# Kernel tuning notes

Hardware: AMD Instinct MI355X
Metric: run time of the kernel (lower is better)

Reference implementation:

```python
import jax, jax.numpy as jnp
import numpy as np

C = 256
CQ = C // 4


def setup_inputs() -> dict:
    key = jax.random.key(0)
    ks = jax.random.split(key, 7)
    B, H, W = 4, 64, 64
    x = jax.random.normal(ks[0], (B, C, H, W), dtype=jnp.float32)
    s = 1.0 / np.sqrt(C)
    Wq = jax.random.normal(ks[1], (CQ, C), dtype=jnp.float32) * s
    bq = jnp.zeros((CQ,), dtype=jnp.float32)
    Wk = jax.random.normal(ks[2], (CQ, C), dtype=jnp.float32) * s
    bk = jnp.zeros((CQ,), dtype=jnp.float32)
    Wv = jax.random.normal(ks[3], (C, C), dtype=jnp.float32) * s
    bv = jnp.zeros((C,), dtype=jnp.float32)
    gamma = jnp.zeros((1,), dtype=jnp.float32)
    return {"x": x, "Wq": Wq, "bq": bq, "Wk": Wk, "bk": bk,
            "Wv": Wv, "bv": bv, "gamma": gamma}


def reference(x, Wq, bq, Wk, bk, Wv, bv, gamma):
    B, Cc, Hh, Ww = x.shape
    N = Hh * Ww
    xf = x.reshape(B, Cc, N)                      # [B, C, N]
    # 1x1 convs are channel-mixing matmuls
    q = jnp.einsum('oc,bcn->bon', Wq, xf) + bq[None, :, None]   # [B, C/4, N]
    k = jnp.einsum('oc,bcn->bon', Wk, xf) + bk[None, :, None]   # [B, C/4, N]
    v = jnp.einsum('oc,bcn->bon', Wv, xf) + bv[None, :, None]   # [B, C, N]
    energy = jnp.einsum('bci,bcj->bij', q, k)     # [B, N, N] (unscaled)
    attn = jax.nn.softmax(energy, axis=-1)
    out = jnp.einsum('bcj,bij->bci', v, attn)     # [B, C, N]
    out = out.reshape(B, Cc, Hh, Ww)
    return gamma[0] * out + x
```

## Files before the change

kernel.cpp:

```cpp
#include <hip/hip_runtime.h>
#include <hip/hip_bf16.h>

typedef unsigned short u16;
typedef unsigned int u32;
typedef float f32x4 __attribute__((ext_vector_type(4)));
typedef short s16x8 __attribute__((ext_vector_type(8)));
typedef short s16x4 __attribute__((ext_vector_type(4)));

#define MFMA16(a, b, c) __builtin_amdgcn_mfma_f32_16x16x32_bf16(a, b, c, 0, 0, 0)

#define NN 4096
#define CC 256
#define CQ 64

__device__ __forceinline__ u16 f2bf(float x) {
    union { float f; u32 u; } v; v.f = x;
    return (u16)((v.u + 0x7FFFu + ((v.u >> 16) & 1u)) >> 16);
}
__device__ __forceinline__ float bf2f(u16 u) {
    union { u32 u; float f; } v; v.u = ((u32)u) << 16;
    return v.f;
}
__device__ __forceinline__ void gll16(const void* g, void* l) {
    __builtin_amdgcn_global_load_lds(
        (const __attribute__((address_space(1))) void*)g,
        (__attribute__((address_space(3))) void*)l, 16, 0, 0);
}

__global__ __launch_bounds__(256) void prep(
    const float* __restrict__ x, const float* __restrict__ Wq,
    const float* __restrict__ Wk, const float* __restrict__ Wv,
    u16* __restrict__ xT, u16* __restrict__ wbf)
{
    const int bid = blockIdx.x, t = threadIdx.x;
    if (bid < 1024) {
        __shared__ float tile[64 * 65];
        const int b = bid >> 8, ctile = (bid >> 6) & 3, ntile = bid & 63;
        const int c0 = ctile * 64, n0 = ntile * 64;
        const int cw = t >> 4, nj = (t & 15) * 4;
        for (int it = 0; it < 4; it++) {
            const int ci = it * 16 + cw;
            const float4 v4 = *(const float4*)(x + ((size_t)(b * CC + c0 + ci)) * NN + n0 + nj);
            tile[(nj + 0) * 65 + ci] = v4.x;
            tile[(nj + 1) * 65 + ci] = v4.y;
            tile[(nj + 2) * 65 + ci] = v4.z;
            tile[(nj + 3) * 65 + ci] = v4.w;
        }
        __syncthreads();
        const int r = t >> 2, c16 = (t & 3) * 16;
        union { u16 h[16]; uint4 q[2]; } pk;
        for (int j = 0; j < 16; j++) pk.h[j] = f2bf(tile[r * 65 + c16 + j]);
        u16* dst = xT + ((size_t)(b * NN + n0 + r)) * CC + c0 + c16;
        *(uint4*)dst = pk.q[0];
        *(uint4*)(dst + 8) = pk.q[1];
    } else {
        const int flat = (bid - 1024) * 1024 + t * 4;
        const int o = flat >> 8, c = flat & 255;
        const float* src = (o < 64)  ? (Wq + (size_t)o * CC + c)
                         : (o < 128) ? (Wk + (size_t)(o - 64) * CC + c)
                                     : (Wv + (size_t)(o - 128) * CC + c);
        const float4 v4 = *(const float4*)src;
        union { u16 h[4]; uint2 d; } pk;
        pk.h[0] = f2bf(v4.x); pk.h[1] = f2bf(v4.y);
        pk.h[2] = f2bf(v4.z); pk.h[3] = f2bf(v4.w);
        *(uint2*)(wbf + (size_t)o * CC + c) = pk.d;
    }
}

__global__ __launch_bounds__(256, 2) void qkv(
    const u16* __restrict__ xT, const u16* __restrict__ wbf,
    const float* __restrict__ bq, const float* __restrict__ bk,
    const float* __restrict__ bv,
    u16* __restrict__ qT, u16* __restrict__ kT, u16* __restrict__ v)
{
    __shared__ __align__(16) u16 sm[384 * 64 + 32 * 64];
    u16* Ws = sm;
    u16* Xs = sm + 384 * 64;

    const int bid = blockIdx.x;
    const int b = bid >> 7, n0 = (bid & 127) * 32;
    const int t = threadIdx.x, lane = t & 63, w = t >> 6;
    const int col = lane & 15, quad = lane >> 4;

    f32x4 acc[6][2];
    for (int i = 0; i < 6; i++) { acc[i][0] = f32x4{0,0,0,0}; acc[i][1] = f32x4{0,0,0,0}; }

    for (int cc = 0; cc < 4; cc++) {
        const int c0 = cc * 64;
        for (int m = 0; m < 12; m++) {
            const int g = w * 768 + m * 64 + lane;
            const int row = g >> 3, ch = g & 7;
            gll16(wbf + (size_t)row * CC + c0 + ((ch ^ (row & 7)) * 8),
                  Ws + (size_t)(w * 768 + m * 64) * 8 + lane * 8);
        }
        {
            const int g = w * 64 + lane;
            const int n = g >> 3, ch = g & 7;
            gll16(xT + ((size_t)(b * NN + n0 + n)) * CC + c0 + ((ch ^ (n & 7)) * 8),
                  Xs + (size_t)(w * 64) * 8 + lane * 8);
        }
        __syncthreads();
        for (int kk = 0; kk < 2; kk++) {
            s16x8 bx[2];
            for (int nt2 = 0; nt2 < 2; nt2++) {
                const int n = nt2 * 16 + col;
                bx[nt2] = *(const s16x8*)&Xs[n * 64 + (((kk * 4 + quad) ^ (n & 7)) * 8)];
            }
            for (int ot = 0; ot < 6; ot++) {
                const int row = w * 96 + ot * 16 + col;
                const s16x8 a = *(const s16x8*)&Ws[row * 64 + (((kk * 4 + quad) ^ (row & 7)) * 8)];
                acc[ot][0] = MFMA16(a, bx[0], acc[ot][0]);
                acc[ot][1] = MFMA16(a, bx[1], acc[ot][1]);
            }
        }
        __syncthreads();
    }
    for (int ot = 0; ot < 6; ot++) {
        const int og = w * 96 + ot * 16 + quad * 4;
        for (int nt2 = 0; nt2 < 2; nt2++) {
            const int n = n0 + nt2 * 16 + col;
            if (og < 64) {
                union { u16 h[4]; uint2 d; } pk;
                for (int r = 0; r < 4; r++) pk.h[r] = f2bf(acc[ot][nt2][r] + bq[og + r]);
                *(uint2*)(qT + ((size_t)(b * NN + n)) * CQ + og) = pk.d;
            } else if (og < 128) {
                union { u16 h[4]; uint2 d; } pk;
                for (int r = 0; r < 4; r++) pk.h[r] = f2bf(acc[ot][nt2][r] + bk[og - 64 + r]);
                *(uint2*)(kT + ((size_t)(b * NN + n)) * CQ + (og - 64)) = pk.d;
            } else {
                for (int r = 0; r < 4; r++)
                    v[((size_t)(b * CC + og - 128 + r)) * NN + n] =
                        f2bf(acc[ot][nt2][r] + bv[og - 128 + r]);
            }
        }
    }
}

__global__ __launch_bounds__(512, 2) void flash_attn(
    const u16* __restrict__ qT, const u16* __restrict__ kT,
    const u16* __restrict__ v, const float* __restrict__ x,
    const float* __restrict__ gamma, float* __restrict__ out)
{
    __shared__ __align__(16) u16 sm[49664];
    __shared__ float ls[2][64];

    const int bid = blockIdx.x;
    const int p = bid & 7;
    const int b = p >> 1;
    const int n0 = ((bid >> 3) + (p & 1) * 32) * 64;
    const int t = threadIdx.x;
    const int lane = t & 63, wv = t >> 6;
    const int col = lane & 15, quad = lane >> 4;
    const int strip = wv & 3, jhalf = wv >> 2;
    const int ih = wv >> 2, cq = wv & 3;

    s16x8 aq[2];
    {
        const u16* qp = qT + ((size_t)(b * NN + n0 + strip * 16 + col)) * CQ + quad * 8;
        aq[0] = *(const s16x8*)qp;
        aq[1] = *(const s16x8*)(qp + 32);
    }

    f32x4 o_[2][4];
    for (int i = 0; i < 2; i++) for (int j = 0; j < 4; j++) o_[i][j] = f32x4{0,0,0,0};
    float l[4] = {0.f, 0.f, 0.f, 0.f};

    const int kg = wv * 64 + lane;
    const int krow = kg >> 3;
    const u16* ksrc = kT + ((size_t)(b * NN + krow)) * CQ + (((kg & 7) ^ (krow & 7)) * 8);
    const int kdo = kg * 8;
    int vgi[4];
    const u16* vsrc[4];
    for (int m = 0; m < 4; m++) {
        const int g = wv * 256 + m * 64 + lane;
        const int row = g >> 3;
        vgi[m] = g * 8;
        vsrc[m] = v + ((size_t)(b * CC + row)) * NN + (((g & 7) ^ (row & 7)) * 8);
    }

    auto issueK = [&](int jt, int kb) {
        gll16(ksrc + (size_t)jt * 64 * CQ, sm + kb * 4096 + kdo);
    };
    auto issueV = [&](int jt, int vb) {
        u16* base = sm + 8192 + vb * 16384;
        for (int m = 0; m < 4; m++)
            gll16(vsrc[m] + jt * 64, base + vgi[m]);
    };
    auto S_phase = [&](int kb, int pb) {
        const u16* Kb = sm + kb * 4096;
        u16* Pb = sm + 40960 + pb * 4352;
        f32x4 s[2] = { f32x4{0,0,0,0}, f32x4{0,0,0,0} };
        for (int kk = 0; kk < 2; kk++)
            for (int jtt = 0; jtt < 2; jtt++) {
                const int jrow = jhalf * 32 + jtt * 16 + col;
                const s16x8 bk_ = *(const s16x8*)
                    &Kb[jrow * 64 + (((kk * 4 + quad) ^ (jrow & 7)) * 8)];
                s[jtt] = MFMA16(aq[kk], bk_, s[jtt]);
            }
        for (int jtt = 0; jtt < 2; jtt++)
            for (int r = 0; r < 4; r++) {
                const float pv = __expf(fminf(s[jtt][r], 60.f));
                l[r] += pv;
                Pb[(strip * 16 + quad * 4 + r) * 68 + jhalf * 32 + jtt * 16 + col] = f2bf(pv);
            }
    };
    auto PV_phase = [&](int pb, int vb) {
        const u16* Pb = sm + 40960 + pb * 4352;
        const u16* Vb = sm + 8192 + vb * 16384;
        for (int kk = 0; kk < 2; kk++) {
            s16x8 pa[2];
            for (int it2 = 0; it2 < 2; it2++) {
                const u16* pp = &Pb[((ih * 2 + it2) * 16 + col) * 68 + kk * 32 + quad * 8];
                const s16x4 lo = *(const s16x4*)pp;
                const s16x4 hi = *(const s16x4*)(pp + 4);
                pa[it2] = s16x8{lo[0], lo[1], lo[2], lo[3], hi[0], hi[1], hi[2], hi[3]};
            }
            for (int ct = 0; ct < 4; ct++) {
                const int c = cq * 64 + ct * 16 + col;
                const s16x8 bv_ = *(const s16x8*)
                    &Vb[c * 64 + (((kk * 4 + quad) ^ (c & 7)) * 8)];
                o_[0][ct] = MFMA16(pa[0], bv_, o_[0][ct]);
                o_[1][ct] = MFMA16(pa[1], bv_, o_[1][ct]);
            }
        }
    };

    issueK(0, 0);
    issueV(0, 0);
    issueK(1, 1);
    __syncthreads();
    S_phase(0, 0);

    int vcur = 0, pcur = 0;
    for (int m = 0; m < 64; m++) {
        __syncthreads();
        issueV((m + 1 < 64) ? m + 1 : 63, vcur ^ 1);
        issueK((m + 2 < 64) ? m + 2 : 63, m & 1);
        PV_phase(pcur, vcur);
        if (m < 63) S_phase((m + 1) & 1, pcur ^ 1);
        vcur ^= 1; pcur ^= 1;
    }

    for (int r = 0; r < 4; r++) {
        float lv = l[r];
        lv += __shfl_xor(lv, 1, 64);
        lv += __shfl_xor(lv, 2, 64);
        lv += __shfl_xor(lv, 4, 64);
        lv += __shfl_xor(lv, 8, 64);
        l[r] = lv;
    }
    if (col == 0)
        for (int r = 0; r < 4; r++)
            ls[jhalf][strip * 16 + quad * 4 + r] = l[r];
    __syncthreads();

    const float g = gamma[0];
    u16* Ts = sm;
    for (int it2 = 0; it2 < 2; it2++) {
        float sc[4];
        for (int r = 0; r < 4; r++) {
            const int irow = (ih * 2 + it2) * 16 + quad * 4 + r;
            sc[r] = g / (ls[0][irow] + ls[1][irow]);
        }
        for (int ct = 0; ct < 4; ct++) {
            const int c = cq * 64 + ct * 16 + col;
            union { u16 h[4]; uint2 d; } pk;
            for (int r = 0; r < 4; r++) pk.h[r] = f2bf(o_[it2][ct][r] * sc[r]);
            *(uint2*)&Ts[c * 72 + (ih * 2 + it2) * 16 + quad * 4] = pk.d;
        }
    }
    __syncthreads();
    for (int it = 0; it < 4; it++) {
        const int c = (t >> 3) + it * 64;
        const int n8 = (t & 7) * 8;
        const u16* os = &Ts[c * 72 + n8];
        const float* xp = x + ((size_t)(b * CC + c)) * NN + n0 + n8;
        float* op = out + ((size_t)(b * CC + c)) * NN + n0 + n8;
        const float4 x0 = *(const float4*)xp;
        const float4 x1 = *(const float4*)(xp + 4);
        float4 r0, r1;
        r0.x = x0.x + bf2f(os[0]); r0.y = x0.y + bf2f(os[1]);
        r0.z = x0.z + bf2f(os[2]); r0.w = x0.w + bf2f(os[3]);
        r1.x = x1.x + bf2f(os[4]); r1.y = x1.y + bf2f(os[5]);
        r1.z = x1.z + bf2f(os[6]); r1.w = x1.w + bf2f(os[7]);
        *(float4*)op = r0;
        *(float4*)(op + 4) = r1;
    }
}

extern "C" void kernel_launch(void* const* d_in, const int* in_sizes, int n_in,
                              void* d_out, int out_size, void* d_ws, size_t ws_size,
                              hipStream_t stream)
{
    const float* x     = (const float*)d_in[0];
    const float* Wq    = (const float*)d_in[1];
    const float* bq    = (const float*)d_in[2];
    const float* Wk    = (const float*)d_in[3];
    const float* bk    = (const float*)d_in[4];
    const float* Wv    = (const float*)d_in[5];
    const float* bv    = (const float*)d_in[6];
    const float* gamma = (const float*)d_in[7];
    float* out = (float*)d_out;

    u16* xT  = (u16*)d_ws;
    u16* wbf = xT  + (size_t)4 * NN * CC;
    u16* qTw = wbf + (size_t)384 * CC;
    u16* kTw = qTw + (size_t)4 * NN * CQ;
    u16* vw  = kTw + (size_t)4 * NN * CQ;

    prep<<<1120, 256, 0, stream>>>(x, Wq, Wk, Wv, xT, wbf);
    qkv<<<512, 256, 0, stream>>>(xT, wbf, bq, bk, bv, qTw, kTw, vw);
    flash_attn<<<256, 512, 0, stream>>>(qTw, kTw, vw, x, gamma, out);
}
```

Baseline: 185.7 us.

## Keep P in registers by transposing S and splitting keys across waves

Reorganizes the attention loop so each wave computes the transposed score tile (keys by queries). The exp'd probabilities then sit directly in the B-operand layout of a 16x16x16 MFMA, which removes the P round-trip through shared memory and one barrier per tile. Key columns are split across four waves, so partial outputs and row sums have to be reduced through shared memory in a serialized four-step epilogue. Other changes: simpler double buffering, a larger accumulator set (32 f32x4 per wave), an fp32 epilogue instead of bf16, and dropping the 2-blocks-per-CU launch bound, which risks lower occupancy.

```diff
diff --git a/kernel.cpp b/kernel.cpp
--- a/kernel.cpp
+++ b/kernel.cpp
@@ -9,6 +9,19 @@
 
 #define MFMA16(a, b, c) __builtin_amdgcn_mfma_f32_16x16x32_bf16(a, b, c, 0, 0, 0)
 
+__device__ __forceinline__ f32x4 mfma_k16(s16x4 a, s16x4 b, f32x4 c) {
+#if __has_builtin(__builtin_amdgcn_mfma_f32_16x16x16_bf16)
+    return __builtin_amdgcn_mfma_f32_16x16x16_bf16(a, b, c, 0, 0, 0);
+#elif __has_builtin(__builtin_amdgcn_mfma_f32_16x16x16bf16_1k)
+    return __builtin_amdgcn_mfma_f32_16x16x16bf16_1k(a, b, c, 0, 0, 0);
+#else
+    f32x4 d;
+    asm volatile("s_nop 1\n\tv_mfma_f32_16x16x16_bf16 %0, %1, %2, %3\n\ts_nop 1"
+                 : "=v"(d) : "v"(a), "v"(b), "v"(c));
+    return d;
+#endif
+}
+
 #define NN 4096
 #define CC 256
 #define CQ 64
@@ -16,10 +29,6 @@
 __device__ __forceinline__ u16 f2bf(float x) {
     union { float f; u32 u; } v; v.f = x;
     return (u16)((v.u + 0x7FFFu + ((v.u >> 16) & 1u)) >> 16);
-}
-__device__ __forceinline__ float bf2f(u16 u) {
-    union { u32 u; float f; } v; v.u = ((u32)u) << 16;
-    return v.f;
 }
 __device__ __forceinline__ void gll16(const void* g, void* l) {
     __builtin_amdgcn_global_load_lds(
@@ -136,13 +145,14 @@
     }
 }
 
-__global__ __launch_bounds__(512, 2) void flash_attn(
+__global__ __launch_bounds__(512) void flash_attn(
     const u16* __restrict__ qT, const u16* __restrict__ kT,
     const u16* __restrict__ v, const float* __restrict__ x,
     const float* __restrict__ gamma, float* __restrict__ out)
 {
-    __shared__ __align__(16) u16 sm[49664];
-    __shared__ float ls[2][64];
+    __shared__ __align__(16) u16 sm[40960];
+    __shared__ __align__(16) float ls[4][64];
+    __shared__ __align__(16) float linv[64];
 
     const int bid = blockIdx.x;
     const int p = bid & 7;
@@ -151,30 +161,28 @@
     const int t = threadIdx.x;
     const int lane = t & 63, wv = t >> 6;
     const int col = lane & 15, quad = lane >> 4;
-    const int strip = wv & 3, jhalf = wv >> 2;
-    const int ih = wv >> 2, cq = wv & 3;
-
-    s16x8 aq[2];
-    {
-        const u16* qp = qT + ((size_t)(b * NN + n0 + strip * 16 + col)) * CQ + quad * 8;
-        aq[0] = *(const s16x8*)qp;
-        aq[1] = *(const s16x8*)(qp + 32);
-    }
-
-    f32x4 o_[2][4];
-    for (int i = 0; i < 2; i++) for (int j = 0; j < 4; j++) o_[i][j] = f32x4{0,0,0,0};
-    float l[4] = {0.f, 0.f, 0.f, 0.f};
-
-    const int kg = wv * 64 + lane;
-    const int krow = kg >> 3;
-    const u16* ksrc = kT + ((size_t)(b * NN + krow)) * CQ + (((kg & 7) ^ (krow & 7)) * 8);
-    const int kdo = kg * 8;
-    int vgi[4];
+    const int jq = wv & 3, ch = wv >> 2;
+
+    s16x8 qfrag[4][2];
+    for (int it = 0; it < 4; it++) {
+        const u16* qp = qT + ((size_t)(b * NN + n0 + it * 16 + col)) * CQ + quad * 8;
+        qfrag[it][0] = *(const s16x8*)qp;
+        qfrag[it][1] = *(const s16x8*)(qp + 32);
+    }
+
+    f32x4 o_[8][4];
+    for (int i = 0; i < 8; i++) for (int j = 0; j < 4; j++) o_[i][j] = f32x4{0,0,0,0};
+    float lac[4] = {0.f, 0.f, 0.f, 0.f};
+
+    const int krow = t >> 3;
+    const u16* ksrc = kT + ((size_t)(b * NN + krow)) * CQ + (((t & 7) ^ (krow & 7)) * 8);
+    const int kdo = t * 8;
     const u16* vsrc[4];
+    int vdo[4];
     for (int m = 0; m < 4; m++) {
-        const int g = wv * 256 + m * 64 + lane;
+        const int g = m * 512 + t;
         const int row = g >> 3;
-        vgi[m] = g * 8;
+        vdo[m] = g * 8;
         vsrc[m] = v + ((size_t)(b * CC + row)) * NN + (((g & 7) ^ (row & 7)) * 8);
     }
 
@@ -184,105 +192,93 @@
     auto issueV = [&](int jt, int vb) {
         u16* base = sm + 8192 + vb * 16384;
         for (int m = 0; m < 4; m++)
-            gll16(vsrc[m] + jt * 64, base + vgi[m]);
-    };
-    auto S_phase = [&](int kb, int pb) {
-        const u16* Kb = sm + kb * 4096;
-        u16* Pb = sm + 40960 + pb * 4352;
-        f32x4 s[2] = { f32x4{0,0,0,0}, f32x4{0,0,0,0} };
-        for (int kk = 0; kk < 2; kk++)
-            for (int jtt = 0; jtt < 2; jtt++) {
-                const int jrow = jhalf * 32 + jtt * 16 + col;
-                const s16x8 bk_ = *(const s16x8*)
-                    &Kb[jrow * 64 + (((kk * 4 + quad) ^ (jrow & 7)) * 8)];
-                s[jtt] = MFMA16(aq[kk], bk_, s[jtt]);
-            }
-        for (int jtt = 0; jtt < 2; jtt++)
-            for (int r = 0; r < 4; r++) {
-                const float pv = __expf(fminf(s[jtt][r], 60.f));
-                l[r] += pv;
-                Pb[(strip * 16 + quad * 4 + r) * 68 + jhalf * 32 + jtt * 16 + col] = f2bf(pv);
-            }
-    };
-    auto PV_phase = [&](int pb, int vb) {
-        const u16* Pb = sm + 40960 + pb * 4352;
-        const u16* Vb = sm + 8192 + vb * 16384;
-        for (int kk = 0; kk < 2; kk++) {
-            s16x8 pa[2];
-            for (int it2 = 0; it2 < 2; it2++) {
-                const u16* pp = &Pb[((ih * 2 + it2) * 16 + col) * 68 + kk * 32 + quad * 8];
-                const s16x4 lo = *(const s16x4*)pp;
-                const s16x4 hi = *(const s16x4*)(pp + 4);
-                pa[it2] = s16x8{lo[0], lo[1], lo[2], lo[3], hi[0], hi[1], hi[2], hi[3]};
-            }
-            for (int ct = 0; ct < 4; ct++) {
-                const int c = cq * 64 + ct * 16 + col;
-                const s16x8 bv_ = *(const s16x8*)
-                    &Vb[c * 64 + (((kk * 4 + quad) ^ (c & 7)) * 8)];
-                o_[0][ct] = MFMA16(pa[0], bv_, o_[0][ct]);
-                o_[1][ct] = MFMA16(pa[1], bv_, o_[1][ct]);
-            }
-        }
+            gll16(vsrc[m] + jt * 64, base + vdo[m]);
     };
 
     issueK(0, 0);
     issueV(0, 0);
-    issueK(1, 1);
     __syncthreads();
-    S_phase(0, 0);
-
-    int vcur = 0, pcur = 0;
+
+    const int c8 = col & 7;
     for (int m = 0; m < 64; m++) {
-        __syncthreads();
-        issueV((m + 1 < 64) ? m + 1 : 63, vcur ^ 1);
-        issueK((m + 2 < 64) ? m + 2 : 63, m & 1);
-        PV_phase(pcur, vcur);
-        if (m < 63) S_phase((m + 1) & 1, pcur ^ 1);
-        vcur ^= 1; pcur ^= 1;
-    }
-
-    for (int r = 0; r < 4; r++) {
-        float lv = l[r];
-        lv += __shfl_xor(lv, 1, 64);
-        lv += __shfl_xor(lv, 2, 64);
-        lv += __shfl_xor(lv, 4, 64);
-        lv += __shfl_xor(lv, 8, 64);
-        l[r] = lv;
-    }
-    if (col == 0)
-        for (int r = 0; r < 4; r++)
-            ls[jhalf][strip * 16 + quad * 4 + r] = l[r];
+        const int cur = m & 1;
+        if (m < 63) { issueK(m + 1, cur ^ 1); issueV(m + 1, cur ^ 1); }
+
+        const u16* Kb = sm + cur * 4096;
+        f32x4 s[4];
+        for (int it = 0; it < 4; it++) s[it] = f32x4{0,0,0,0};
+        for (int kk = 0; kk < 2; kk++) {
+            const s16x8 a = *(const s16x8*)
+                &Kb[(jq * 16 + col) * 64 + (((kk * 4 + quad) ^ c8) * 8)];
+            for (int it = 0; it < 4; it++)
+                s[it] = MFMA16(a, qfrag[it][kk], s[it]);
+        }
+        s16x4 pfrag[4];
+        for (int it = 0; it < 4; it++) {
+            union { u16 h[4]; s16x4 v4; } pk;
+            for (int r = 0; r < 4; r++) {
+                const float pv = __expf(fminf(s[it][r], 60.f));
+                lac[it] += pv;
+                pk.h[r] = f2bf(pv);
+            }
+            pfrag[it] = pk.v4;
+        }
+        const u16* Vb = sm + 8192 + cur * 16384;
+        const int lch = jq * 2 + (quad >> 1), sub = (quad & 1) * 4;
+        for (int ct = 0; ct < 8; ct++) {
+            const int c = ch * 128 + ct * 16 + col;
+            const s16x4 va = *(const s16x4*)&Vb[c * 64 + ((lch ^ c8) * 8) + sub];
+            for (int it = 0; it < 4; it++)
+                o_[ct][it] = mfma_k16(va, pfrag[it], o_[ct][it]);
+        }
+        __syncthreads();
+    }
+
+    for (int it = 0; it < 4; it++) {
+        float lv = lac[it];
+        lv += __shfl_xor(lv, 16, 64);
+        lv += __shfl_xor(lv, 32, 64);
+        lac[it] = lv;
+    }
+    if (ch == 0 && quad == 0)
+        for (int it = 0; it < 4; it++) ls[jq][it * 16 + col] = lac[it];
+
+    float* F = (float*)sm;
+    const int fb = ch * 8704;
+    for (int s = 0; s < 4; s++) {
+        __syncthreads();
+        if (jq == s) {
+            for (int ct = 0; ct < 8; ct++)
+                for (int it = 0; it < 4; it++)
+                    for (int r = 0; r < 4; r++) {
+                        const int addr = fb + (ct * 16 + quad * 4 + r) * 68 + it * 16 + col;
+                        if (s == 0) F[addr] = o_[ct][it][r];
+                        else        F[addr] += o_[ct][it][r];
+                    }
+        }
+    }
     __syncthreads();
-
-    const float g = gamma[0];
-    u16* Ts = sm;
-    for (int it2 = 0; it2 < 2; it2++) {
-        float sc[4];
-        for (int r = 0; r < 4; r++) {
-            const int irow = (ih * 2 + it2) * 16 + quad * 4 + r;
-            sc[r] = g / (ls[0][irow] + ls[1][irow]);
-        }
-        for (int ct = 0; ct < 4; ct++) {
-            const int c = cq * 64 + ct * 16 + col;
-            union { u16 h[4]; uint2 d; } pk;
-            for (int r = 0; r < 4; r++) pk.h[r] = f2bf(o_[it2][ct][r] * sc[r]);
-            *(uint2*)&Ts[c * 72 + (ih * 2 + it2) * 16 + quad * 4] = pk.d;
-        }
-    }
+    if (t < 64)
+        linv[t] = gamma[0] / (ls[0][t] + ls[1][t] + ls[2][t] + ls[3][t]);
     __syncthreads();
+
     for (int it = 0; it < 4; it++) {
         const int c = (t >> 3) + it * 64;
         const int n8 = (t & 7) * 8;
-        const u16* os = &Ts[c * 72 + n8];
+        const float* Fr = F + (c >> 7) * 8704 + (c & 127) * 68 + n8;
+        const float4 l0 = *(const float4*)&linv[n8];
+        const float4 l1 = *(const float4*)&linv[n8 + 4];
+        const float4 f0 = *(const float4*)Fr;
+        const float4 f1 = *(const float4*)(Fr + 4);
         const float* xp = x + ((size_t)(b * CC + c)) * NN + n0 + n8;
         float* op = out + ((size_t)(b * CC + c)) * NN + n0 + n8;
         const float4 x0 = *(const float4*)xp;
         const float4 x1 = *(const float4*)(xp + 4);
         float4 r0, r1;
-        r0.x = x0.x + bf2f(os[0]); r0.y = x0.y + bf2f(os[1]);
-        r0.z = x0.z + bf2f(os[2]); r0.w = x0.w + bf2f(os[3]);
-        r1.x = x1.x + bf2f(os[4]); r1.y = x1.y + bf2f(os[5]);
-        r1.z = x1.z + bf2f(os[6]); r1.w = x1.w + bf2f(os[7]);
+        r0.x = x0.x + f0.x * l0.x; r0.y = x0.y + f0.y * l0.y;
+        r0.z = x0.z + f0.z * l0.z; r0.w = x0.w + f0.w * l0.w;
+        r1.x = x1.x + f1.x * l1.x; r1.y = x1.y + f1.y * l1.y;
+        r1.z = x1.z + f1.z * l1.z; r1.w = x1.w + f1.w * l1.w;
         *(float4*)op = r0;
         *(float4*)(op + 4) = r1;
     }
```

New measurement: 228.8 us. 1.23x slower.

## Split attention keys across two blocks per query tile and combine partials

Applied to the files above, without the earlier changes.

The flash attention kernel now splits the key range into two halves handled by separate blocks. This doubles the grid to 512 blocks, halves the K/V tile size and shared memory per block, and raises the occupancy hint. Each half writes unnormalized partial outputs (one in bf16, one in fp32) and row sums to workspace. A new combine kernel merges them with the residual and gamma scaling. The qkv kernel also moves to 512 threads with fewer accumulators per wave. The split adds extra global traffic for the partial outputs and a fourth kernel launch, in exchange for more parallelism across the CUs.

```diff
diff --git a/kernel.cpp b/kernel.cpp
--- a/kernel.cpp
+++ b/kernel.cpp
@@ -5,7 +5,6 @@
 typedef unsigned int u32;
 typedef float f32x4 __attribute__((ext_vector_type(4)));
 typedef short s16x8 __attribute__((ext_vector_type(8)));
-typedef short s16x4 __attribute__((ext_vector_type(4)));
 
 #define MFMA16(a, b, c) __builtin_amdgcn_mfma_f32_16x16x32_bf16(a, b, c, 0, 0, 0)
 
@@ -67,7 +66,7 @@
     }
 }
 
-__global__ __launch_bounds__(256, 2) void qkv(
+__global__ __launch_bounds__(512, 4) void qkv(
     const u16* __restrict__ xT, const u16* __restrict__ wbf,
     const float* __restrict__ bq, const float* __restrict__ bk,
     const float* __restrict__ bv,
@@ -82,22 +81,21 @@
     const int t = threadIdx.x, lane = t & 63, w = t >> 6;
     const int col = lane & 15, quad = lane >> 4;
 
-    f32x4 acc[6][2];
-    for (int i = 0; i < 6; i++) { acc[i][0] = f32x4{0,0,0,0}; acc[i][1] = f32x4{0,0,0,0}; }
+    f32x4 acc[3][2];
+    for (int i = 0; i < 3; i++) { acc[i][0] = f32x4{0,0,0,0}; acc[i][1] = f32x4{0,0,0,0}; }
 
     for (int cc = 0; cc < 4; cc++) {
         const int c0 = cc * 64;
-        for (int m = 0; m < 12; m++) {
-            const int g = w * 768 + m * 64 + lane;
+        for (int m = 0; m < 6; m++) {
+            const int g = m * 512 + t;
             const int row = g >> 3, ch = g & 7;
-            gll16(wbf + (size_t)row * CC + c0 + ((ch ^ (row & 7)) * 8),
-                  Ws + (size_t)(w * 768 + m * 64) * 8 + lane * 8);
-        }
-        {
+            gll16(wbf + (size_t)row * CC + c0 + ((ch ^ (row & 7)) * 8), Ws + g * 8);
+        }
+        if (w < 4) {
             const int g = w * 64 + lane;
             const int n = g >> 3, ch = g & 7;
             gll16(xT + ((size_t)(b * NN + n0 + n)) * CC + c0 + ((ch ^ (n & 7)) * 8),
-                  Xs + (size_t)(w * 64) * 8 + lane * 8);
+                  Xs + g * 8);
         }
         __syncthreads();
         for (int kk = 0; kk < 2; kk++) {
@@ -106,8 +104,8 @@
                 const int n = nt2 * 16 + col;
                 bx[nt2] = *(const s16x8*)&Xs[n * 64 + (((kk * 4 + quad) ^ (n & 7)) * 8)];
             }
-            for (int ot = 0; ot < 6; ot++) {
-                const int row = w * 96 + ot * 16 + col;
+            for (int ot = 0; ot < 3; ot++) {
+                const int row = w * 48 + ot * 16 + col;
                 const s16x8 a = *(const s16x8*)&Ws[row * 64 + (((kk * 4 + quad) ^ (row & 7)) * 8)];
                 acc[ot][0] = MFMA16(a, bx[0], acc[ot][0]);
                 acc[ot][1] = MFMA16(a, bx[1], acc[ot][1]);
@@ -115,8 +113,8 @@
         }
         __syncthreads();
     }
-    for (int ot = 0; ot < 6; ot++) {
-        const int og = w * 96 + ot * 16 + quad * 4;
+    for (int ot = 0; ot < 3; ot++) {
+        const int og = w * 48 + ot * 16 + quad * 4;
         for (int nt2 = 0; nt2 < 2; nt2++) {
             const int n = n0 + nt2 * 16 + col;
             if (og < 64) {
@@ -136,22 +134,24 @@
     }
 }
 
-__global__ __launch_bounds__(512, 2) void flash_attn(
+__global__ __launch_bounds__(512, 4) void flash_attn(
     const u16* __restrict__ qT, const u16* __restrict__ kT,
-    const u16* __restrict__ v, const float* __restrict__ x,
-    const float* __restrict__ gamma, float* __restrict__ out)
-{
-    __shared__ __align__(16) u16 sm[49664];
+    const u16* __restrict__ v,
+    u16* __restrict__ Op0, float* __restrict__ Op1,
+    float* __restrict__ lws)
+{
+    __shared__ __align__(16) u16 sm[25600];
     __shared__ float ls[2][64];
 
     const int bid = blockIdx.x;
     const int p = bid & 7;
-    const int b = p >> 1;
-    const int n0 = ((bid >> 3) + (p & 1) * 32) * 64;
+    const int b = p >> 1, jh = p & 1;
+    const int n0 = (bid >> 3) * 64;
+    const int jb = jh * 2048;
     const int t = threadIdx.x;
     const int lane = t & 63, wv = t >> 6;
     const int col = lane & 15, quad = lane >> 4;
-    const int strip = wv & 3, jhalf = wv >> 2;
+    const int strip = wv & 3, jhi = wv >> 2;
     const int ih = wv >> 2, cq = wv & 3;
 
     s16x8 aq[2];
@@ -163,65 +163,56 @@
 
     f32x4 o_[2][4];
     for (int i = 0; i < 2; i++) for (int j = 0; j < 4; j++) o_[i][j] = f32x4{0,0,0,0};
-    float l[4] = {0.f, 0.f, 0.f, 0.f};
+    float lac[4] = {0.f, 0.f, 0.f, 0.f};
 
     const int kg = wv * 64 + lane;
     const int krow = kg >> 3;
-    const u16* ksrc = kT + ((size_t)(b * NN + krow)) * CQ + (((kg & 7) ^ (krow & 7)) * 8);
+    const u16* ksrc = kT + ((size_t)(b * NN + jb + krow)) * CQ + (((kg & 7) ^ (krow & 7)) * 8);
     const int kdo = kg * 8;
-    int vgi[4];
-    const u16* vsrc[4];
-    for (int m = 0; m < 4; m++) {
-        const int g = wv * 256 + m * 64 + lane;
-        const int row = g >> 3;
-        vgi[m] = g * 8;
-        vsrc[m] = v + ((size_t)(b * CC + row)) * NN + (((g & 7) ^ (row & 7)) * 8);
+    const u16* vsrc[2];
+    int vdo[2];
+    for (int m = 0; m < 2; m++) {
+        const int g = m * 512 + t;
+        const int row = g >> 2;
+        vdo[m] = g * 8;
+        vsrc[m] = v + ((size_t)(b * CC + row)) * NN + jb + (g & 3) * 8;
     }
 
     auto issueK = [&](int jt, int kb) {
-        gll16(ksrc + (size_t)jt * 64 * CQ, sm + kb * 4096 + kdo);
+        if (wv < 4) gll16(ksrc + (size_t)jt * 32 * CQ, sm + kb * 2048 + kdo);
     };
     auto issueV = [&](int jt, int vb) {
-        u16* base = sm + 8192 + vb * 16384;
-        for (int m = 0; m < 4; m++)
-            gll16(vsrc[m] + jt * 64, base + vgi[m]);
+        u16* base = sm + 4096 + vb * 8192;
+        for (int m = 0; m < 2; m++)
+            gll16(vsrc[m] + jt * 32, base + vdo[m]);
     };
     auto S_phase = [&](int kb, int pb) {
-        const u16* Kb = sm + kb * 4096;
-        u16* Pb = sm + 40960 + pb * 4352;
-        f32x4 s[2] = { f32x4{0,0,0,0}, f32x4{0,0,0,0} };
-        for (int kk = 0; kk < 2; kk++)
-            for (int jtt = 0; jtt < 2; jtt++) {
-                const int jrow = jhalf * 32 + jtt * 16 + col;
-                const s16x8 bk_ = *(const s16x8*)
-                    &Kb[jrow * 64 + (((kk * 4 + quad) ^ (jrow & 7)) * 8)];
-                s[jtt] = MFMA16(aq[kk], bk_, s[jtt]);
-            }
-        for (int jtt = 0; jtt < 2; jtt++)
-            for (int r = 0; r < 4; r++) {
-                const float pv = __expf(fminf(s[jtt][r], 60.f));
-                l[r] += pv;
-                Pb[(strip * 16 + quad * 4 + r) * 68 + jhalf * 32 + jtt * 16 + col] = f2bf(pv);
-            }
+        const u16* Kb = sm + kb * 2048;
+        u16* Pb = sm + 20480 + pb * 2560;
+        f32x4 s = f32x4{0,0,0,0};
+        for (int kk = 0; kk < 2; kk++) {
+            const int jrow = jhi * 16 + col;
+            const s16x8 bk_ = *(const s16x8*)
+                &Kb[jrow * 64 + (((kk * 4 + quad) ^ (jrow & 7)) * 8)];
+            s = MFMA16(aq[kk], bk_, s);
+        }
+        for (int r = 0; r < 4; r++) {
+            const float pv = __expf(fminf(s[r], 60.f));
+            lac[r] += pv;
+            Pb[(strip * 16 + quad * 4 + r) * 40 + jhi * 16 + col] = f2bf(pv);
+        }
     };
     auto PV_phase = [&](int pb, int vb) {
-        const u16* Pb = sm + 40960 + pb * 4352;
-        const u16* Vb = sm + 8192 + vb * 16384;
-        for (int kk = 0; kk < 2; kk++) {
-            s16x8 pa[2];
-            for (int it2 = 0; it2 < 2; it2++) {
-                const u16* pp = &Pb[((ih * 2 + it2) * 16 + col) * 68 + kk * 32 + quad * 8];
-                const s16x4 lo = *(const s16x4*)pp;
-                const s16x4 hi = *(const s16x4*)(pp + 4);
-                pa[it2] = s16x8{lo[0], lo[1], lo[2], lo[3], hi[0], hi[1], hi[2], hi[3]};
-            }
-            for (int ct = 0; ct < 4; ct++) {
-                const int c = cq * 64 + ct * 16 + col;
-                const s16x8 bv_ = *(const s16x8*)
-                    &Vb[c * 64 + (((kk * 4 + quad) ^ (c & 7)) * 8)];
-                o_[0][ct] = MFMA16(pa[0], bv_, o_[0][ct]);
-                o_[1][ct] = MFMA16(pa[1], bv_, o_[1][ct]);
-            }
+        const u16* Pb = sm + 20480 + pb * 2560;
+        const u16* Vb = sm + 4096 + vb * 8192;
+        s16x8 pa[2];
+        for (int it2 = 0; it2 < 2; it2++)
+            pa[it2] = *(const s16x8*)&Pb[((ih * 2 + it2) * 16 + col) * 40 + quad * 8];
+        for (int ct = 0; ct < 4; ct++) {
+            const int c = cq * 64 + ct * 16 + col;
+            const s16x8 bv_ = *(const s16x8*)&Vb[c * 32 + quad * 8];
+            o_[0][ct] = MFMA16(pa[0], bv_, o_[0][ct]);
+            o_[1][ct] = MFMA16(pa[1], bv_, o_[1][ct]);
         }
     };
 
@@ -242,50 +233,76 @@
     }
 
     for (int r = 0; r < 4; r++) {
-        float lv = l[r];
+        float lv = lac[r];
         lv += __shfl_xor(lv, 1, 64);
         lv += __shfl_xor(lv, 2, 64);
         lv += __shfl_xor(lv, 4, 64);
         lv += __shfl_xor(lv, 8, 64);
-        l[r] = lv;
+        lac[r] = lv;
     }
     if (col == 0)
         for (int r = 0; r < 4; r++)
-            ls[jhalf][strip * 16 + quad * 4 + r] = l[r];
+            ls[jhi][strip * 16 + quad * 4 + r] = lac[r];
     __syncthreads();
-
+    if (t < 64)
+        lws[(size_t)jh * 4 * NN + (size_t)b * NN + n0 + t] = ls[0][t] + ls[1][t];
+
+    float* Tf = (float*)sm;
+    u16*  Tu = sm;
+    for (int rd = 0; rd < 2; rd++) {
+        if ((cq >> 1) == rd) {
+            const int cl = (cq & 1) * 64;
+            for (int it2 = 0; it2 < 2; it2++) {
+                const int ib = (ih * 2 + it2) * 16 + quad * 4;
+                for (int ct = 0; ct < 4; ct++) {
+                    const int c = cl + ct * 16 + col;
+                    if (jh == 0) {
+                        union { u16 h[4]; uint2 d; } pk;
+                        for (int r = 0; r < 4; r++) pk.h[r] = f2bf(o_[it2][ct][r]);
+                        *(uint2*)&Tu[c * 136 + ib] = pk.d;
+                    } else {
+                        *(float2*)&Tf[c * 68 + ib] = float2{o_[it2][ct][0], o_[it2][ct][1]};
+                        *(float2*)&Tf[c * 68 + ib + 2] = float2{o_[it2][ct][2], o_[it2][ct][3]};
+                    }
+                }
+            }
+        }
+        __syncthreads();
+        const int cl = t >> 2, i0 = (t & 3) * 16;
+        const int c = rd * 128 + cl;
+        if (jh == 0) {
+            u16* dst = Op0 + ((size_t)(b * CC + c)) * NN + n0 + i0;
+            *(uint4*)dst       = *(const uint4*)&Tu[cl * 136 + i0];
+            *(uint4*)(dst + 8) = *(const uint4*)&Tu[cl * 136 + i0 + 8];
+        } else {
+            float* dst = Op1 + ((size_t)(b * CC + c)) * NN + n0 + i0;
+            for (int k = 0; k < 4; k++)
+                *(float4*)(dst + k * 4) = *(const float4*)&Tf[cl * 68 + i0 + k * 4];
+        }
+        __syncthreads();
+    }
+}
+
+__global__ __launch_bounds__(256) void combine(
+    const float* __restrict__ x, const u16* __restrict__ Op0,
+    const float* __restrict__ lws, const float* __restrict__ gamma,
+    float* __restrict__ out)
+{
+    const size_t idx = ((size_t)blockIdx.x * 256 + threadIdx.x) * 4;
+    const int b = (int)(idx >> 20);
+    const int n = (int)(idx & (NN - 1));
     const float g = gamma[0];
-    u16* Ts = sm;
-    for (int it2 = 0; it2 < 2; it2++) {
-        float sc[4];
-        for (int r = 0; r < 4; r++) {
-            const int irow = (ih * 2 + it2) * 16 + quad * 4 + r;
-            sc[r] = g / (ls[0][irow] + ls[1][irow]);
-        }
-        for (int ct = 0; ct < 4; ct++) {
-            const int c = cq * 64 + ct * 16 + col;
-            union { u16 h[4]; uint2 d; } pk;
-            for (int r = 0; r < 4; r++) pk.h[r] = f2bf(o_[it2][ct][r] * sc[r]);
-            *(uint2*)&Ts[c * 72 + (ih * 2 + it2) * 16 + quad * 4] = pk.d;
-        }
-    }
-    __syncthreads();
-    for (int it = 0; it < 4; it++) {
-        const int c = (t >> 3) + it * 64;
-        const int n8 = (t & 7) * 8;
-        const u16* os = &Ts[c * 72 + n8];
-        const float* xp = x + ((size_t)(b * CC + c)) * NN + n0 + n8;
-        float* op = out + ((size_t)(b * CC + c)) * NN + n0 + n8;
-        const float4 x0 = *(const float4*)xp;
-        const float4 x1 = *(const float4*)(xp + 4);
-        float4 r0, r1;
-        r0.x = x0.x + bf2f(os[0]); r0.y = x0.y + bf2f(os[1]);
-        r0.z = x0.z + bf2f(os[2]); r0.w = x0.w + bf2f(os[3]);
-        r1.x = x1.x + bf2f(os[4]); r1.y = x1.y + bf2f(os[5]);
-        r1.z = x1.z + bf2f(os[6]); r1.w = x1.w + bf2f(os[7]);
-        *(float4*)op = r0;
-        *(float4*)(op + 4) = r1;
-    }
+    const float4 xv = *(const float4*)(x + idx);
+    const float4 o1 = *(const float4*)(out + idx);
+    const u16* o0p = Op0 + idx;
+    const float4 l0 = *(const float4*)(lws + (size_t)b * NN + n);
+    const float4 l1 = *(const float4*)(lws + (size_t)4 * NN + (size_t)b * NN + n);
+    float4 r;
+    r.x = xv.x + g * (bf2f(o0p[0]) + o1.x) / (l0.x + l1.x);
+    r.y = xv.y + g * (bf2f(o0p[1]) + o1.y) / (l0.y + l1.y);
+    r.z = xv.z + g * (bf2f(o0p[2]) + o1.z) / (l0.z + l1.z);
+    r.w = xv.w + g * (bf2f(o0p[3]) + o1.w) / (l0.w + l1.w);
+    *(float4*)(out + idx) = r;
 }
 
 extern "C" void kernel_launch(void* const* d_in, const int* in_sizes, int n_in,
@@ -307,8 +324,11 @@
     u16* qTw = wbf + (size_t)384 * CC;
     u16* kTw = qTw + (size_t)4 * NN * CQ;
     u16* vw  = kTw + (size_t)4 * NN * CQ;
+    u16* Op0 = xT;
+    float* lws = (float*)wbf;
 
     prep<<<1120, 256, 0, stream>>>(x, Wq, Wk, Wv, xT, wbf);
-    qkv<<<512, 256, 0, stream>>>(xT, wbf, bq, bk, bv, qTw, kTw, vw);
-    flash_attn<<<256, 512, 0, stream>>>(qTw, kTw, vw, x, gamma, out);
-}
+    qkv<<<512, 512, 0, stream>>>(xT, wbf, bq, bk, bv, qTw, kTw, vw);
+    flash_attn<<<512, 512, 0, stream>>>(qTw, kTw, vw, Op0, out, lws);
+    combine<<<4096, 256, 0, stream>>>(x, Op0, lws, gamma, out);
+}
```

New measurement: 169.9 us. 8.5% less time.
